# Kernel optimization log

Hardware: AMD Instinct MI355X
Metric: run time of the kernel (lower is better)

The kernel has to match this reference:

```python
import jax, jax.numpy as jnp
import numpy as np

N_SRC = 100000
N_TGT = 100000
N_EDGES = 1600000
D = 128
HID = 128
OUT = 64
NUM_LAYERS = 2
P_DROP = 0.1
NEG_SLOPE = 0.01


def setup_inputs() -> dict:
    key = jax.random.key(0)
    ks = jax.random.split(key, 16)
    s = 1.0 / np.sqrt(D)
    inp = {
        "x_source": jax.random.normal(ks[0], (N_SRC, D), jnp.float32),
        "x_target": jax.random.normal(ks[1], (N_TGT, D), jnp.float32),
        "Wl_tgt": jax.random.normal(ks[2], (NUM_LAYERS, D, HID), jnp.float32) * s,
        "bl_tgt": jax.random.normal(ks[3], (NUM_LAYERS, HID), jnp.float32) * s,
        "Wr_tgt": jax.random.normal(ks[4], (NUM_LAYERS, D, HID), jnp.float32) * s,
        "Wl_src": jax.random.normal(ks[5], (NUM_LAYERS, D, HID), jnp.float32) * s,
        "bl_src": jax.random.normal(ks[6], (NUM_LAYERS, HID), jnp.float32) * s,
        "Wr_src": jax.random.normal(ks[7], (NUM_LAYERS, D, HID), jnp.float32) * s,
        "W_out": jax.random.normal(ks[8], (HID, OUT), jnp.float32) * (1.0 / np.sqrt(HID)),
        "b_out": jax.random.normal(ks[9], (OUT,), jnp.float32) * 0.01,
        "edge_src": jax.random.randint(ks[10], (N_EDGES,), 0, N_SRC, jnp.int32),
        "edge_dst": jax.random.randint(ks[11], (N_EDGES,), 0, N_TGT, jnp.int32),
        "rev_src": jax.random.randint(ks[12], (N_EDGES,), 0, N_TGT, jnp.int32),
        "rev_dst": jax.random.randint(ks[13], (N_EDGES,), 0, N_SRC, jnp.int32),
    }
    return inp


def _sage(x_src, x_dst, src_idx, dst_idx, n_dst, Wl, bl, Wr):
    # mean-aggregate neighbor messages per destination node (PyG SAGEConv default)
    msg = x_src[src_idx]  # [E, D] gather
    agg = jax.ops.segment_sum(msg, dst_idx, num_segments=n_dst)  # [n_dst, D]
    cnt = jax.ops.segment_sum(jnp.ones((src_idx.shape[0],), msg.dtype), dst_idx,
                              num_segments=n_dst)
    mean = agg / jnp.maximum(cnt, 1.0)[:, None]
    return mean @ Wl + bl + x_dst @ Wr


def _dropout(x, key):
    keep = jax.random.bernoulli(key, 1.0 - P_DROP, x.shape)
    return jnp.where(keep, x / (1.0 - P_DROP), jnp.zeros((), x.dtype))


def reference(x_source, x_target, Wl_tgt, bl_tgt, Wr_tgt, Wl_src, bl_src, Wr_src,
              W_out, b_out, edge_src, edge_dst, rev_src, rev_dst):
    dkey = jax.random.key(42)
    xs, xt = x_source, x_target
    for l in range(NUM_LAYERS):
        # ('source','edge','target'): target receives from source
        new_t = _sage(xs, xt, edge_src, edge_dst, N_TGT, Wl_tgt[l], bl_tgt[l], Wr_tgt[l])
        # ('target','rev_edge','source'): source receives from target
        new_s = _sage(xt, xs, rev_src, rev_dst, N_SRC, Wl_src[l], bl_src[l], Wr_src[l])
        new_t = jax.nn.leaky_relu(new_t, NEG_SLOPE)
        new_s = jax.nn.leaky_relu(new_s, NEG_SLOPE)
        new_t = _dropout(new_t, jax.random.fold_in(dkey, 2 * l))
        new_s = _dropout(new_s, jax.random.fold_in(dkey, 2 * l + 1))
        xs, xt = new_s, new_t
    return xs @ W_out + b_out
```

## Files before the change

### kernel.cpp

```cpp
#include <hip/hip_runtime.h>
#include <stdint.h>

#define NN 100000
#define NE 1600000
#define DD 128
#define G8 12544
#define SUBN 98
#define NND 100352
#define RCAP 2304
#define NBIN 2048
#define HBH 256
#define SB2 512

typedef unsigned short u16;
typedef unsigned long long u64;
typedef short short8 __attribute__((ext_vector_type(8)));
typedef float floatx4 __attribute__((ext_vector_type(4)));
typedef float floatx2 __attribute__((ext_vector_type(2)));
typedef int intx4 __attribute__((ext_vector_type(4)));

__device__ static inline u16 f2bf(float f){
  unsigned u = __float_as_uint(f);
  unsigned r = u + 0x7FFFu + ((u >> 16) & 1u);
  return (u16)(r >> 16);
}

__host__ __device__ static inline unsigned rotl32(unsigned x, int r){
  return (x << r) | (x >> (32 - r));
}

__host__ __device__ static inline void tf2x32(unsigned k0, unsigned k1,
                                              unsigned c0, unsigned c1,
                                              unsigned &o0, unsigned &o1)
{
  const unsigned ks2 = k0 ^ k1 ^ 0x1BD11BDAu;
  unsigned x0 = c0 + k0, x1 = c1 + k1;
#define TFR(r) { x0 += x1; x1 = rotl32(x1, (r)); x1 ^= x0; }
  TFR(13) TFR(15) TFR(26) TFR(6)   x0 += k1;  x1 += ks2 + 1u;
  TFR(17) TFR(29) TFR(16) TFR(24)  x0 += ks2; x1 += k0 + 2u;
  TFR(13) TFR(15) TFR(26) TFR(6)   x0 += k0;  x1 += k1 + 3u;
  TFR(17) TFR(29) TFR(16) TFR(24)  x0 += k1;  x1 += ks2 + 4u;
  TFR(13) TFR(15) TFR(26) TFR(6)   x0 += ks2; x1 += k0 + 5u;
#undef TFR
  o0 = x0; o1 = x1;
}

__device__ static inline int drop_keep(unsigned k0, unsigned k1, unsigned j)
{
  unsigned o0, o1;
  tf2x32(k0, k1, 0u, j, o0, o1);
  const unsigned bits = o0 ^ o1;
  const float u = __uint_as_float((bits >> 9) | 0x3F800000u) - 1.0f;
  return u < 0.9f;
}

__device__ static inline void acc4(floatx2 &p0, floatx2 &p1, floatx2 &p2,
                                   floatx2 &p3, uint4 v){
  floatx2 t0, t1, t2, t3;
  t0[0] = __uint_as_float(v.x << 16); t0[1] = __uint_as_float(v.x & 0xFFFF0000u);
  t1[0] = __uint_as_float(v.y << 16); t1[1] = __uint_as_float(v.y & 0xFFFF0000u);
  t2[0] = __uint_as_float(v.z << 16); t2[1] = __uint_as_float(v.z & 0xFFFF0000u);
  t3[0] = __uint_as_float(v.w << 16); t3[1] = __uint_as_float(v.w & 0xFFFF0000u);
  p0 += t0; p1 += t1; p2 += t2; p3 += t3;
}

__device__ static inline int dbin(int dir, int d, int &nl){
  int g = d / G8;
  nl = d - g * G8;
  return (dir << 10) | (g << 7) | (nl / SUBN);
}

#define CVB 12500
__global__ __launch_bounds__(256) void k_pre(
    const float* __restrict__ ina, const float* __restrict__ inb,
    u16* __restrict__ oa, u16* __restrict__ ob, int n8,
    const int* __restrict__ e_dst, const int* __restrict__ r_dst,
    int* __restrict__ histg,
    const float* __restrict__ Wl_tgt, const float* __restrict__ Wr_tgt,
    const float* __restrict__ Wl_src, const float* __restrict__ Wr_src,
    const float* __restrict__ Wo,
    u16* __restrict__ Wsw0, u16* __restrict__ Wsw1, u16* __restrict__ Wsw2,
    u16* __restrict__ Wswo)
{
  const int blk = blockIdx.x;
  const int t = threadIdx.x;
  if (blk < CVB){
    int i = blk * 256 + t;
    const float* in = ina; u16* out = oa;
    if (i >= n8){ i -= n8; in = inb; out = ob; }
    floatx4 a = __builtin_nontemporal_load((const floatx4*)in + (size_t)i * 2);
    floatx4 c = __builtin_nontemporal_load((const floatx4*)in + (size_t)i * 2 + 1);
    u16 v[8] = { f2bf(a[0]), f2bf(a[1]), f2bf(a[2]), f2bf(a[3]),
                 f2bf(c[0]), f2bf(c[1]), f2bf(c[2]), f2bf(c[3]) };
    *(uint4*)(out + (size_t)i * 8) = *(const uint4*)v;
  } else if (blk < CVB + HBH){
    const int hb = blk - CVB;
    __shared__ int h2[NBIN];
    for (int i = t; i < NBIN; i += 256) h2[i] = 0;
    __syncthreads();
    const int QT = 2 * (NE / 4);
    for (int i = hb * 256 + t; i < QT; i += HBH * 256){
      int dir = (i >= NE / 4);
      int qi = dir ? i - NE / 4 : i;
      const int* dp = dir ? r_dst : e_dst;
      intx4 d = __builtin_nontemporal_load((const intx4*)dp + qi);
      int nl;
      atomicAdd(&h2[dbin(dir, d.x, nl)], 1);
      atomicAdd(&h2[dbin(dir, d.y, nl)], 1);
      atomicAdd(&h2[dbin(dir, d.z, nl)], 1);
      atomicAdd(&h2[dbin(dir, d.w, nl)], 1);
    }
    __syncthreads();
    for (int i = t; i < NBIN; i += 256){
      int c = h2[i];
      if (c) atomicAdd(&histg[i], c);
    }
  } else {
    int b = blk - CVB - HBH;
    if (b < 48){
      const float *Wl, *Wr; u16* dst;
      if (b < 16){ Wl = Wl_tgt; Wr = Wr_tgt; dst = Wsw0; }
      else if (b < 32){ Wl = Wl_src; Wr = Wr_src; dst = Wsw1; b -= 16; }
      else { Wl = Wl_src + 16384; Wr = Wr_src + 16384; dst = Wsw2; b -= 32; }
      int idx = b * 256 + t;
      int lane = idx & 63, tile = idx >> 6;
      int kt = tile >> 3, nt = tile & 7;
      int n = nt * 16 + (lane & 15);
      int kb = kt * 32 + (lane >> 4) * 8;
      u16 v[8];
      #pragma unroll
      for (int j = 0; j < 8; ++j){
        int k = kb + j;
        float w = (k < 128) ? Wl[(size_t)k * 128 + n] : Wr[(size_t)(k - 128) * 128 + n];
        v[j] = f2bf(w);
      }
      *(uint4*)(dst + (size_t)idx * 8) = *(const uint4*)v;
    } else {
      int idx = (b - 48) * 256 + t;
      int lane = idx & 63, tile = idx >> 6;
      int kt = tile >> 2, nt = tile & 3;
      int n = nt * 16 + (lane & 15);
      int kb = kt * 32 + (lane >> 4) * 8;
      u16 v[8];
      #pragma unroll
      for (int j = 0; j < 8; ++j)
        v[j] = f2bf(Wo[(size_t)(kb + j) * 64 + n]);
      *(uint4*)(Wswo + (size_t)idx * 8) = *(const uint4*)v;
    }
  }
}

__global__ __launch_bounds__(256) void k_scan2(const int* __restrict__ histg,
                                               int* __restrict__ base2,
                                               int* __restrict__ gcur){
  __shared__ int tot[256];
  const int t = threadIdx.x;
  int v[8]; int s = 0;
  #pragma unroll
  for (int j = 0; j < 8; ++j){ v[j] = s; s += histg[t * 8 + j]; }
  tot[t] = s;
  __syncthreads();
  int mine = s;
  for (int off = 1; off < 256; off <<= 1){
    int u = (t >= off) ? tot[t - off] : 0;
    __syncthreads();
    tot[t] += u;
    __syncthreads();
  }
  int run = tot[t] - mine;
  #pragma unroll
  for (int j = 0; j < 8; ++j){
    base2[t * 8 + j] = run + v[j];
    gcur[t * 8 + j]  = run + v[j];
  }
  if (t == 0) base2[NBIN] = 2 * NE;
}

__global__ __launch_bounds__(256) void k_scat(const int* __restrict__ e_src,
                                              const int* __restrict__ e_dst,
                                              const int* __restrict__ r_src,
                                              const int* __restrict__ r_dst,
                                              int* __restrict__ gcur,
                                              unsigned* __restrict__ stage){
  __shared__ intx4 dq[7 * 256];
  __shared__ int lcnt[NBIN], lbase[NBIN], lcur[NBIN];
  const int t = threadIdx.x;
  const int QT = 2 * (NE / 4);
  for (int i = t; i < NBIN; i += 256) lcnt[i] = 0;
  __syncthreads();
  {
    int j = 0;
    for (int i = blockIdx.x * 256 + t; i < QT; i += SB2 * 256, ++j){
      int dir = (i >= NE / 4);
      int qi = dir ? i - NE / 4 : i;
      const int* dp = dir ? r_dst : e_dst;
      intx4 d = __builtin_nontemporal_load((const intx4*)dp + qi);
      dq[j * 256 + t] = d;
      int nl;
      atomicAdd(&lcnt[dbin(dir, d.x, nl)], 1);
      atomicAdd(&lcnt[dbin(dir, d.y, nl)], 1);
      atomicAdd(&lcnt[dbin(dir, d.z, nl)], 1);
      atomicAdd(&lcnt[dbin(dir, d.w, nl)], 1);
    }
  }
  __syncthreads();
  for (int i = t; i < NBIN; i += 256){
    int c = lcnt[i];
    lbase[i] = c ? atomicAdd(&gcur[i], c) : 0;
    lcur[i] = 0;
  }
  __syncthreads();
  {
    int j = 0;
    for (int i = blockIdx.x * 256 + t; i < QT; i += SB2 * 256, ++j){
      int dir = (i >= NE / 4);
      int qi = dir ? i - NE / 4 : i;
      const int* sp = dir ? r_src : e_src;
      intx4 s = __builtin_nontemporal_load((const intx4*)sp + qi);
      intx4 d = dq[j * 256 + t];
      int nl, b, p;
      b = dbin(dir, d.x, nl); p = lbase[b] + atomicAdd(&lcur[b], 1);
      stage[p] = (unsigned)s.x | ((unsigned)nl << 17);
      b = dbin(dir, d.y, nl); p = lbase[b] + atomicAdd(&lcur[b], 1);
      stage[p] = (unsigned)s.y | ((unsigned)nl << 17);
      b = dbin(dir, d.z, nl); p = lbase[b] + atomicAdd(&lcur[b], 1);
      stage[p] = (unsigned)s.z | ((unsigned)nl << 17);
      b = dbin(dir, d.w, nl); p = lbase[b] + atomicAdd(&lcur[b], 1);
      stage[p] = (unsigned)s.w | ((unsigned)nl << 17);
    }
  }
}

__global__ __launch_bounds__(256) void k_fill4(const unsigned* __restrict__ stage,
                                               const int* __restrict__ base2,
                                               int* __restrict__ ptr,
                                               int* __restrict__ csr){
  __shared__ unsigned rec[RCAP];
  __shared__ unsigned srt[RCAP];
  __shared__ int ldeg[SUBN], lptr[SUBN], lcur[SUBN];
  const int sb = blockIdx.x;
  const int b16 = sb >> 7, sub = sb & 127;
  const int dir = b16 >> 3, g = b16 & 7;
  const int t = threadIdx.x;
  const int beg = base2[sb];
  const int end = base2[sb + 1];
  int n = end - beg;
  if (n > RCAP) n = RCAP;
  for (int i = t; i < n; i += 256) rec[i] = stage[beg + i];
  if (t < SUBN) ldeg[t] = 0;
  __syncthreads();
  const int nl0 = sub * SUBN;
  for (int i = t; i < n; i += 256)
    atomicAdd(&ldeg[(int)(rec[i] >> 17) - nl0], 1);
  __syncthreads();
  if (t == 0){
    int run = 0;
    for (int s = 0; s < SUBN; ++s){ lptr[s] = run; lcur[s] = run; run += ldeg[s]; }
  }
  __syncthreads();
  for (int i = t; i < n; i += 256){
    int rl = (int)(rec[i] >> 17) - nl0;
    int pos = atomicAdd(&lcur[rl], 1);
    srt[pos] = rec[i] & 0x1FFFFu;
  }
  __syncthreads();
  const int node0 = g * G8 + nl0;
  if (t < SUBN) ptr[dir * NND + node0 + t] = beg + lptr[t];
  if (sb == 2047 && t == 0) ptr[2 * NND] = 2 * NE;
  for (int i = t; i < n; i += 256) csr[beg + i] = (int)srt[i];
}

template<bool WM>
__device__ static inline void agg_body(const u16* __restrict__ x,
                                       const int* __restrict__ pd,
                                       const int* __restrict__ csr,
                                       u16* __restrict__ out,
                                       u64* __restrict__ msk,
                                       unsigned key0, unsigned key1, int blk){
  const int row = blk * 4 + (threadIdx.x >> 6);
  const int lane = threadIdx.x & 63;
  const int sub = lane >> 4, l4 = lane & 15;
  const int beg = pd[row], end = pd[row + 1];
  const int cnt = end - beg;
  floatx2 p0 = (floatx2)0.f, p1 = (floatx2)0.f, p2 = (floatx2)0.f, p3 = (floatx2)0.f;
  int e = 0;
  for (; e + 15 < cnt; e += 16){
    int s0 = csr[beg + e + sub];
    int s1 = csr[beg + e + 4 + sub];
    int s2 = csr[beg + e + 8 + sub];
    int s3 = csr[beg + e + 12 + sub];
    uint4 v0 = *(const uint4*)(x + (size_t)s0 * DD + l4 * 8);
    uint4 v1 = *(const uint4*)(x + (size_t)s1 * DD + l4 * 8);
    uint4 v2 = *(const uint4*)(x + (size_t)s2 * DD + l4 * 8);
    uint4 v3 = *(const uint4*)(x + (size_t)s3 * DD + l4 * 8);
    acc4(p0, p1, p2, p3, v0);
    acc4(p0, p1, p2, p3, v1);
    acc4(p0, p1, p2, p3, v2);
    acc4(p0, p1, p2, p3, v3);
  }
  for (; e + 7 < cnt; e += 8){
    int s0 = csr[beg + e + sub];
    int s1 = csr[beg + e + 4 + sub];
    uint4 v0 = *(const uint4*)(x + (size_t)s0 * DD + l4 * 8);
    uint4 v1 = *(const uint4*)(x + (size_t)s1 * DD + l4 * 8);
    acc4(p0, p1, p2, p3, v0);
    acc4(p0, p1, p2, p3, v1);
  }
  for (; e + 3 < cnt; e += 4){
    int s0 = csr[beg + e + sub];
    uint4 v0 = *(const uint4*)(x + (size_t)s0 * DD + l4 * 8);
    acc4(p0, p1, p2, p3, v0);
  }
  if (e + sub < cnt){
    int s0 = csr[beg + e + sub];
    uint4 v0 = *(const uint4*)(x + (size_t)s0 * DD + l4 * 8);
    acc4(p0, p1, p2, p3, v0);
  }
  if (WM){
    u64 mA = __ballot(drop_keep(key0, key1, (unsigned)row * 128u + (unsigned)lane));
    u64 mB = __ballot(drop_keep(key0, key1, (unsigned)row * 128u + 64u + (unsigned)lane));
    if (lane < 2) msk[(size_t)row * 2 + lane] = lane ? mB : mA;
  }
  float a[8] = { p0[0], p0[1], p1[0], p1[1], p2[0], p2[1], p3[0], p3[1] };
  #pragma unroll
  for (int i = 0; i < 8; ++i){
    a[i] += __shfl_xor(a[i], 16);
    a[i] += __shfl_xor(a[i], 32);
  }
  const float inv = (cnt > 0) ? (1.0f / (float)cnt) : 1.0f;
  if (sub == 0){
    unsigned pk[4];
    #pragma unroll
    for (int i = 0; i < 4; ++i)
      pk[i] = (unsigned)f2bf(a[2*i] * inv) | ((unsigned)f2bf(a[2*i+1] * inv) << 16);
    *(uint4*)(out + (size_t)row * DD + l4 * 8) = make_uint4(pk[0], pk[1], pk[2], pk[3]);
  }
}

__global__ __launch_bounds__(256) void k_aggD(const u16* __restrict__ x0,
    const u16* __restrict__ x1, const int* __restrict__ ptr,
    const int* __restrict__ csr, u16* __restrict__ o0, u16* __restrict__ o1,
    u64* __restrict__ m0, u64* __restrict__ m1,
    unsigned k00, unsigned k01, unsigned k10, unsigned k11){
  int b = blockIdx.x;
  if (b < NN / 4) agg_body<true>(x0, ptr, csr, o0, m0, k00, k01, b);
  else            agg_body<true>(x1, ptr + NND, csr, o1, m1, k10, k11, b - NN / 4);
}

__global__ __launch_bounds__(256) void k_agg1(const u16* __restrict__ x,
    const int* __restrict__ ptr, const int* __restrict__ csr,
    u16* __restrict__ out, u64* __restrict__ msk,
    unsigned key0, unsigned key1){
  agg_body<true>(x, ptr + NND, csr, out, msk, key0, key1, blockIdx.x);
}

__device__ static inline void fused_body(const u16* __restrict__ Am,
    const u16* __restrict__ X, const u16* __restrict__ Wsw,
    const float* __restrict__ bias, u16* __restrict__ outH,
    const u64* __restrict__ msk, int blk)
{
  const int wave = threadIdx.x >> 6, lane = threadIdx.x & 63;
  const int quad = lane >> 4, col0 = lane & 15;
  const int row0 = blk * 64 + wave * 16;
  int m = row0 + col0;
  if (m >= NN) m = NN - 1;

  floatx4 acc[8];
  #pragma unroll
  for (int i = 0; i < 8; ++i) acc[i] = (floatx4)0.f;

  #pragma unroll
  for (int kt = 0; kt < 8; ++kt){
    const int k = kt * 32 + quad * 8;
    const u16* ap = (k < 128) ? (Am + (size_t)m * 128 + k)
                              : (X  + (size_t)m * 128 + (k - 128));
    short8 a = __builtin_nontemporal_load((const short8*)ap);
    #pragma unroll
    for (int nt = 0; nt < 8; ++nt){
      short8 b = *(const short8*)(Wsw + (size_t)(((kt * 8 + nt) * 64 + lane) * 8));
      acc[nt] = __builtin_amdgcn_mfma_f32_16x16x32_bf16(a, b, acc[nt], 0, 0, 0);
    }
  }

  u64 w0[4], w1[4];
  #pragma unroll
  for (int rg = 0; rg < 4; ++rg){
    int r = row0 + quad * 4 + rg;
    size_t rr = (size_t)((r < NN) ? r : (NN - 1)) * 2;
    w0[rg] = msk[rr];
    w1[rg] = msk[rr + 1];
  }

  #pragma unroll
  for (int nt = 0; nt < 8; ++nt){
    const int col = nt * 16 + col0;
    const float bj = bias[col];
    const int sh = col & 63;
    #pragma unroll
    for (int rg = 0; rg < 4; ++rg){
      const int r = row0 + quad * 4 + rg;
      if (r < NN){
        float h = acc[nt][rg] + bj;
        h = (h >= 0.f) ? h : 0.01f * h;
        u64 w = (nt < 4) ? w0[rg] : w1[rg];
        h = ((w >> sh) & 1ull) ? h * (1.0f / 0.9f) : 0.0f;
        outH[(size_t)r * 128 + col] = f2bf(h);
      }
    }
  }
}

#define GB ((NN + 63) / 64)

__global__ __launch_bounds__(256) void k_fusedD(
    const u16* __restrict__ A0, const u16* __restrict__ X0,
    const u16* __restrict__ W0, const float* __restrict__ b0,
    u16* __restrict__ o0, const u64* __restrict__ m0,
    const u16* __restrict__ A1, const u16* __restrict__ X1,
    const u16* __restrict__ W1, const float* __restrict__ b1,
    u16* __restrict__ o1, const u64* __restrict__ m1)
{
  int b = blockIdx.x;
  if (b < GB) fused_body(A0, X0, W0, b0, o0, m0, b);
  else        fused_body(A1, X1, W1, b1, o1, m1, b - GB);
}

__global__ __launch_bounds__(256) void k_fused(const u16* __restrict__ Am,
    const u16* __restrict__ X, const u16* __restrict__ Wsw,
    const float* __restrict__ bias, u16* __restrict__ outH,
    const u64* __restrict__ msk)
{
  fused_body(Am, X, Wsw, bias, outH, msk, blockIdx.x);
}

__global__ __launch_bounds__(256) void k_out(const u16* __restrict__ H,
    const u16* __restrict__ Wsw, const float* __restrict__ bias,
    float* __restrict__ out)
{
  const int wave = threadIdx.x >> 6, lane = threadIdx.x & 63;
  const int quad = lane >> 4, col0 = lane & 15;
  const int row0 = blockIdx.x * 64 + wave * 16;
  int m = row0 + col0;
  if (m >= NN) m = NN - 1;

  floatx4 acc[4];
  #pragma unroll
  for (int i = 0; i < 4; ++i) acc[i] = (floatx4)0.f;

  #pragma unroll
  for (int kt = 0; kt < 4; ++kt){
    short8 a = __builtin_nontemporal_load(
        (const short8*)(H + (size_t)m * 128 + kt * 32 + quad * 8));
    #pragma unroll
    for (int nt = 0; nt < 4; ++nt){
      short8 b = *(const short8*)(Wsw + (size_t)(((kt * 4 + nt) * 64 + lane) * 8));
      acc[nt] = __builtin_amdgcn_mfma_f32_16x16x32_bf16(a, b, acc[nt], 0, 0, 0);
    }
  }

  #pragma unroll
  for (int nt = 0; nt < 4; ++nt){
    const int col = nt * 16 + col0;
    const float bj = bias[col];
    #pragma unroll
    for (int rg = 0; rg < 4; ++rg){
      const int r = row0 + quad * 4 + rg;
      if (r < NN)
        out[(size_t)r * 64 + col] = acc[nt][rg] + bj;
    }
  }
}

extern "C" void kernel_launch(void* const* d_in, const int* in_sizes, int n_in,
                              void* d_out, int out_size, void* d_ws, size_t ws_size,
                              hipStream_t stream)
{
  const float* x_src  = (const float*)d_in[0];
  const float* x_tgt  = (const float*)d_in[1];
  const float* Wl_tgt = (const float*)d_in[2];
  const float* bl_tgt = (const float*)d_in[3];
  const float* Wr_tgt = (const float*)d_in[4];
  const float* Wl_src = (const float*)d_in[5];
  const float* bl_src = (const float*)d_in[6];
  const float* Wr_src = (const float*)d_in[7];
  const float* W_o    = (const float*)d_in[8];
  const float* b_o    = (const float*)d_in[9];
  const int*   e_src  = (const int*)d_in[10];
  const int*   e_dst  = (const int*)d_in[11];
  const int*   r_src  = (const int*)d_in[12];
  const int*   r_dst  = (const int*)d_in[13];
  float* out = (float*)d_out;
  (void)in_sizes; (void)n_in; (void)out_size; (void)ws_size;

  char* ws = (char*)d_ws;
  size_t off = 0;
  auto alloc = [&](size_t bytes) -> char* {
    char* p = ws + off; off += (bytes + 255) & ~(size_t)255; return p;
  };
  unsigned* stage = (unsigned*)alloc((size_t)2 * NE * 8);
  u16* A_t  = (u16*)stage;
  u16* A_s  = (u16*)alloc((size_t)NN * DD * 2);
  u16* Xs   = (u16*)alloc((size_t)NN * DD * 2);
  u16* Xt   = (u16*)alloc((size_t)NN * DD * 2);
  u16* B    = (u16*)alloc((size_t)NN * DD * 2);
  u16* C    = (u16*)alloc((size_t)NN * DD * 2);
  u16* Wsw0 = (u16*)alloc(256 * 128 * 2);
  u16* Wsw1 = (u16*)alloc(256 * 128 * 2);
  u16* Wsw2 = (u16*)alloc(256 * 128 * 2);
  u16* Wswo = (u16*)alloc(128 * 64 * 2);
  int* csr  = (int*)alloc((size_t)2 * NE * 4);
  int* ptr  = (int*)alloc((size_t)(2 * NND + 1) * 4);
  int* histg = (int*)alloc((size_t)NBIN * 4);
  int* base2 = (int*)alloc((size_t)(NBIN + 1) * 4);
  int* gcur  = (int*)alloc((size_t)NBIN * 4);
  u64* M0t  = (u64*)alloc((size_t)NN * 2 * 8);
  u64* M0s  = (u64*)alloc((size_t)NN * 2 * 8);
  u64* M1s  = (u64*)alloc((size_t)NN * 2 * 8);

  unsigned kt0a, kt0b, ks0a, ks0b, ks1a, ks1b;
  tf2x32(0u, 42u, 0u, 0u, kt0a, kt0b);
  tf2x32(0u, 42u, 0u, 1u, ks0a, ks0b);
  tf2x32(0u, 42u, 0u, 3u, ks1a, ks1b);

  hipMemsetAsync(histg, 0, (size_t)NBIN * 4, stream);
  k_pre<<<CVB + HBH + 52, 256, 0, stream>>>(x_src, x_tgt, Xs, Xt, NN * DD / 8,
                                            e_dst, r_dst, histg,
                                            Wl_tgt, Wr_tgt, Wl_src, Wr_src, W_o,
                                            Wsw0, Wsw1, Wsw2, Wswo);
  k_scan2<<<1, 256, 0, stream>>>(histg, base2, gcur);
  k_scat<<<SB2, 256, 0, stream>>>(e_src, e_dst, r_src, r_dst, gcur, stage);
  k_fill4<<<2048, 256, 0, stream>>>(stage, base2, ptr, csr);

  const int AB = NN / 4;
  k_aggD<<<2 * AB, 256, 0, stream>>>(Xs, Xt, ptr, csr, A_t, A_s,
                                     M0t, M0s, kt0a, kt0b, ks0a, ks0b);
  k_fusedD<<<2 * GB, 256, 0, stream>>>(A_t, Xt, Wsw0, bl_tgt, B, M0t,
                                       A_s, Xs, Wsw1, bl_src, C, M0s);
  k_agg1<<<AB, 256, 0, stream>>>(B, ptr, csr, A_t, M1s, ks1a, ks1b);
  k_fused<<<GB, 256, 0, stream>>>(A_t, C, Wsw2, bl_src + 128, B, M1s);
  k_out<<<GB, 256, 0, stream>>>(B, Wswo, b_o, out);
}
```

Baseline: 550.9 us.

## Rework edge scatter staging, drop 16-wide agg unroll, hoist mask loads

The scatter kernel no longer caches dst indices in LDS between its counting and placing passes. It re-reads them from global memory in the second pass, reuses lcnt for the block bases, and doubles the grid (SB2). The aggregation body loses its 16-edge unrolled loop, leaving 8/4/remainder loops. The fused GEMM loads dropout mask words before the MFMA loop so their latency overlaps compute. The aim is lower LDS use and higher occupancy in scatter plus better latency hiding, at the cost of a second global read of dst indices and less memory-level parallelism in the aggregation gather.

```diff
diff --git a/kernel.cpp b/kernel.cpp
--- a/kernel.cpp
+++ b/kernel.cpp
@@ -10,7 +10,7 @@
 #define RCAP 2304
 #define NBIN 2048
 #define HBH 256
-#define SB2 512
+#define SB2 1024
 
 typedef unsigned short u16;
 typedef unsigned long long u64;
@@ -182,52 +182,45 @@
                                               const int* __restrict__ r_dst,
                                               int* __restrict__ gcur,
                                               unsigned* __restrict__ stage){
-  __shared__ intx4 dq[7 * 256];
-  __shared__ int lcnt[NBIN], lbase[NBIN], lcur[NBIN];
+  __shared__ int lcnt[NBIN], lcur[NBIN];
   const int t = threadIdx.x;
   const int QT = 2 * (NE / 4);
   for (int i = t; i < NBIN; i += 256) lcnt[i] = 0;
   __syncthreads();
-  {
-    int j = 0;
-    for (int i = blockIdx.x * 256 + t; i < QT; i += SB2 * 256, ++j){
-      int dir = (i >= NE / 4);
-      int qi = dir ? i - NE / 4 : i;
-      const int* dp = dir ? r_dst : e_dst;
-      intx4 d = __builtin_nontemporal_load((const intx4*)dp + qi);
-      dq[j * 256 + t] = d;
-      int nl;
-      atomicAdd(&lcnt[dbin(dir, d.x, nl)], 1);
-      atomicAdd(&lcnt[dbin(dir, d.y, nl)], 1);
-      atomicAdd(&lcnt[dbin(dir, d.z, nl)], 1);
-      atomicAdd(&lcnt[dbin(dir, d.w, nl)], 1);
-    }
+  for (int i = blockIdx.x * 256 + t; i < QT; i += SB2 * 256){
+    int dir = (i >= NE / 4);
+    int qi = dir ? i - NE / 4 : i;
+    const int* dp = dir ? r_dst : e_dst;
+    intx4 d = __builtin_nontemporal_load((const intx4*)dp + qi);
+    int nl;
+    atomicAdd(&lcnt[dbin(dir, d.x, nl)], 1);
+    atomicAdd(&lcnt[dbin(dir, d.y, nl)], 1);
+    atomicAdd(&lcnt[dbin(dir, d.z, nl)], 1);
+    atomicAdd(&lcnt[dbin(dir, d.w, nl)], 1);
   }
   __syncthreads();
   for (int i = t; i < NBIN; i += 256){
     int c = lcnt[i];
-    lbase[i] = c ? atomicAdd(&gcur[i], c) : 0;
+    lcnt[i] = c ? atomicAdd(&gcur[i], c) : 0;
     lcur[i] = 0;
   }
   __syncthreads();
-  {
-    int j = 0;
-    for (int i = blockIdx.x * 256 + t; i < QT; i += SB2 * 256, ++j){
-      int dir = (i >= NE / 4);
-      int qi = dir ? i - NE / 4 : i;
-      const int* sp = dir ? r_src : e_src;
-      intx4 s = __builtin_nontemporal_load((const intx4*)sp + qi);
-      intx4 d = dq[j * 256 + t];
-      int nl, b, p;
-      b = dbin(dir, d.x, nl); p = lbase[b] + atomicAdd(&lcur[b], 1);
-      stage[p] = (unsigned)s.x | ((unsigned)nl << 17);
-      b = dbin(dir, d.y, nl); p = lbase[b] + atomicAdd(&lcur[b], 1);
-      stage[p] = (unsigned)s.y | ((unsigned)nl << 17);
-      b = dbin(dir, d.z, nl); p = lbase[b] + atomicAdd(&lcur[b], 1);
-      stage[p] = (unsigned)s.z | ((unsigned)nl << 17);
-      b = dbin(dir, d.w, nl); p = lbase[b] + atomicAdd(&lcur[b], 1);
-      stage[p] = (unsigned)s.w | ((unsigned)nl << 17);
-    }
+  for (int i = blockIdx.x * 256 + t; i < QT; i += SB2 * 256){
+    int dir = (i >= NE / 4);
+    int qi = dir ? i - NE / 4 : i;
+    const int* dp = dir ? r_dst : e_dst;
+    const int* sp = dir ? r_src : e_src;
+    intx4 d = *((const intx4*)dp + qi);
+    intx4 s = __builtin_nontemporal_load((const intx4*)sp + qi);
+    int nl, b, p;
+    b = dbin(dir, d.x, nl); p = lcnt[b] + atomicAdd(&lcur[b], 1);
+    stage[p] = (unsigned)s.x | ((unsigned)nl << 17);
+    b = dbin(dir, d.y, nl); p = lcnt[b] + atomicAdd(&lcur[b], 1);
+    stage[p] = (unsigned)s.y | ((unsigned)nl << 17);
+    b = dbin(dir, d.z, nl); p = lcnt[b] + atomicAdd(&lcur[b], 1);
+    stage[p] = (unsigned)s.z | ((unsigned)nl << 17);
+    b = dbin(dir, d.w, nl); p = lcnt[b] + atomicAdd(&lcur[b], 1);
+    stage[p] = (unsigned)s.w | ((unsigned)nl << 17);
   }
 }
 
@@ -284,20 +277,6 @@
   const int cnt = end - beg;
   floatx2 p0 = (floatx2)0.f, p1 = (floatx2)0.f, p2 = (floatx2)0.f, p3 = (floatx2)0.f;
   int e = 0;
-  for (; e + 15 < cnt; e += 16){
-    int s0 = csr[beg + e + sub];
-    int s1 = csr[beg + e + 4 + sub];
-    int s2 = csr[beg + e + 8 + sub];
-    int s3 = csr[beg + e + 12 + sub];
-    uint4 v0 = *(const uint4*)(x + (size_t)s0 * DD + l4 * 8);
-    uint4 v1 = *(const uint4*)(x + (size_t)s1 * DD + l4 * 8);
-    uint4 v2 = *(const uint4*)(x + (size_t)s2 * DD + l4 * 8);
-    uint4 v3 = *(const uint4*)(x + (size_t)s3 * DD + l4 * 8);
-    acc4(p0, p1, p2, p3, v0);
-    acc4(p0, p1, p2, p3, v1);
-    acc4(p0, p1, p2, p3, v2);
-    acc4(p0, p1, p2, p3, v3);
-  }
   for (; e + 7 < cnt; e += 8){
     int s0 = csr[beg + e + sub];
     int s1 = csr[beg + e + 4 + sub];
@@ -364,6 +343,15 @@
   const int row0 = blk * 64 + wave * 16;
   int m = row0 + col0;
   if (m >= NN) m = NN - 1;
+
+  u64 w0[4], w1[4];
+  #pragma unroll
+  for (int rg = 0; rg < 4; ++rg){
+    int r = row0 + quad * 4 + rg;
+    size_t rr = (size_t)((r < NN) ? r : (NN - 1)) * 2;
+    w0[rg] = msk[rr];
+    w1[rg] = msk[rr + 1];
+  }
 
   floatx4 acc[8];
   #pragma unroll
@@ -380,15 +368,6 @@
       short8 b = *(const short8*)(Wsw + (size_t)(((kt * 8 + nt) * 64 + lane) * 8));
       acc[nt] = __builtin_amdgcn_mfma_f32_16x16x32_bf16(a, b, acc[nt], 0, 0, 0);
     }
-  }
-
-  u64 w0[4], w1[4];
-  #pragma unroll
-  for (int rg = 0; rg < 4; ++rg){
-    int r = row0 + quad * 4 + rg;
-    size_t rr = (size_t)((r < NN) ? r : (NN - 1)) * 2;
-    w0[rg] = msk[rr];
-    w1[rg] = msk[rr + 1];
   }
 
   #pragma unroll
```

After: 596.8 us. 8.3% more time.
